# Kernel optimization log

Hardware: AMD Instinct MI355X
Metric: run time of the kernel (lower is better)

Reference implementation:

```python
import jax, jax.numpy as jnp
import numpy as np

EPS = 1e-5
NUM_HEADS = 8
POOL_K = 50
POOL_S = 15
DEPTH = 4


def _conv2d(x, w, b, pad_h, pad_w):
    y = jax.lax.conv_general_dilated(
        x, w, window_strides=(1, 1),
        padding=((pad_h, pad_h), (pad_w, pad_w)),
        dimension_numbers=('NCHW', 'OIHW', 'NCHW'))
    return y + b[None, :, None, None]


def _bn_eval(x, g, b):
    # eval-mode BatchNorm2d with running_mean=0, running_var=1
    s = g / jnp.sqrt(1.0 + EPS)
    return x * s[None, :, None, None] + b[None, :, None, None]


def _layernorm(x, g, b):
    m = x.mean(-1, keepdims=True)
    v = ((x - m) ** 2).mean(-1, keepdims=True)
    return (x - m) / jnp.sqrt(v + EPS) * g + b


def _mha(x, wq, bq, wk, bk, wv, bv, wo, bo):
    B, n, d = x.shape
    def split(h):
        return h.reshape(B, n, NUM_HEADS, -1).transpose(0, 2, 1, 3)  # b h n dk
    q = split(x @ wq.T + bq)
    k = split(x @ wk.T + bk)
    v = split(x @ wv.T + bv)
    dk = q.shape[-1]
    scores = jnp.einsum('bhqd,bhkd->bhqk', q, k) / jnp.sqrt(jnp.float32(dk))
    attn = jax.nn.softmax(scores, axis=-1)
    o = jnp.einsum('bhqk,bhkd->bhqd', attn, v).transpose(0, 2, 1, 3).reshape(B, n, d)
    return o @ wo.T + bo


def _encoder(x, p):
    (g1, b1, g2, b2, wq, bq, wk, bk, wv, bv, wo, bo, f1w, f1b, f2w, f2b) = p
    h = _layernorm(x, g1, b1)
    x = x + _mha(h, wq, bq, wk, bk, wv, bv, wo, bo)
    h = _layernorm(x, g2, b2)
    ff = jax.nn.gelu(h @ f1w.T + f1b, approximate=False) @ f2w.T + f2b
    return x + ff


def _forward(x, tw1, tb1, tw2, tb2, tw3, tb3, tw4, tb4, bn1_g, bn1_b, sw, sb,
             bn2_g, bn2_b, ln1_g, ln1_b, ln2_g, ln2_b, wq, bq, wk, bk, wv, bv,
             wo, bo, f1w, f1b, f2w, f2b, ew, eb, bn3_g, bn3_b, cw, cb):
    B, C, T = x.shape
    xi = x[:, None]  # [B,1,C,T]
    h = jnp.concatenate([
        _conv2d(xi, tw1, tb1, 0, 7),
        _conv2d(xi, tw2, tb2, 0, 12),
        _conv2d(xi, tw3, tb3, 0, 25),
        _conv2d(xi, tw4, tb4, 0, 32)], axis=1)          # [B,D,C,T]
    h = _bn_eval(h, bn1_g, bn1_b)
    h = _conv2d(h, sw, sb, 0, 0)                         # [B,D,1,T]
    h = jax.nn.elu(_bn_eval(h, bn2_g, bn2_b))[:, :, 0]   # [B,D,T]

    npos = (T - POOL_K) // POOL_S + 1
    idx = np.arange(npos)[:, None] * POOL_S + np.arange(POOL_K)  # [n,K]
    win = h[:, :, idx]                                   # [B,D,n,K]
    avg = win.mean(-1)                                   # [B,D,n]
    var = win.var(-1, ddof=1)                            # unbiased, like torch
    vlog = jnp.log(jnp.clip(var, 1e-6, 1e6))
    x1 = avg.transpose(0, 2, 1)                          # [B,n,D]
    x2 = vlog.transpose(0, 2, 1)

    for i in range(DEPTH):
        p = (ln1_g[i], ln1_b[i], ln2_g[i], ln2_b[i], wq[i], bq[i], wk[i], bk[i],
             wv[i], bv[i], wo[i], bo[i], f1w[i], f1b[i], f2w[i], f2b[i])
        x1 = _encoder(x1, p)
        x2 = _encoder(x2, p)

    h = jnp.concatenate([x1[:, :, None, :], x2[:, :, None, :]], axis=2)  # [B,n,2,D]
    h = jax.nn.elu(_bn_eval(_conv2d(h, ew, eb, 0, 0), bn3_g, bn3_b))     # [B,n,1,D]
    return h.reshape(B, -1) @ cw.T + cb


def setup_inputs() -> dict:
    B, C, T, D, n, ff, ncls = 16, 64, 1000, 128, 64, 512, 4
    ks = iter(jax.random.split(jax.random.key(0), 48))
    def nrm(shape, s=0.02):
        return jax.random.normal(next(ks), shape, jnp.float32) * s
    inp = {
        'x': jax.random.normal(next(ks), (B, C, T), jnp.float32),
        'tw1': nrm((D // 4, 1, 1, 15)), 'tb1': jnp.zeros(D // 4),
        'tw2': nrm((D // 4, 1, 1, 25)), 'tb2': jnp.zeros(D // 4),
        'tw3': nrm((D // 4, 1, 1, 51)), 'tb3': jnp.zeros(D // 4),
        'tw4': nrm((D // 4, 1, 1, 65)), 'tb4': jnp.zeros(D // 4),
        'bn1_g': jnp.ones(D), 'bn1_b': jnp.zeros(D),
        'sw': nrm((D, D, C, 1)), 'sb': jnp.zeros(D),
        'bn2_g': jnp.ones(D), 'bn2_b': jnp.zeros(D),
        'ln1_g': jnp.ones((DEPTH, D)), 'ln1_b': jnp.zeros((DEPTH, D)),
        'ln2_g': jnp.ones((DEPTH, D)), 'ln2_b': jnp.zeros((DEPTH, D)),
        'wq': nrm((DEPTH, D, D)), 'bq': jnp.zeros((DEPTH, D)),
        'wk': nrm((DEPTH, D, D)), 'bk': jnp.zeros((DEPTH, D)),
        'wv': nrm((DEPTH, D, D)), 'bv': jnp.zeros((DEPTH, D)),
        'wo': nrm((DEPTH, D, D)), 'bo': jnp.zeros((DEPTH, D)),
        'f1w': nrm((DEPTH, ff, D)), 'f1b': jnp.zeros((DEPTH, ff)),
        'f2w': nrm((DEPTH, D, ff)), 'f2b': jnp.zeros((DEPTH, D)),
        'ew': nrm((n, n, 2, 1)), 'eb': jnp.zeros(n),
        'bn3_g': jnp.ones(n), 'bn3_b': jnp.zeros(n),
        'cw': nrm((ncls, D * n)), 'cb': jnp.zeros(ncls),
    }
    return inp


def reference(x, tw1, tb1, tw2, tb2, tw3, tb3, tw4, tb4, bn1_g, bn1_b, sw, sb,
              bn2_g, bn2_b, ln1_g, ln1_b, ln2_g, ln2_b, wq, bq, wk, bk, wv, bv,
              wo, bo, f1w, f1b, f2w, f2b, ew, eb, bn3_g, bn3_b, cw, cb):
    return _forward(x, tw1, tb1, tw2, tb2, tw3, tb3, tw4, tb4, bn1_g, bn1_b,
                    sw, sb, bn2_g, bn2_b, ln1_g, ln1_b, ln2_g, ln2_b, wq, bq,
                    wk, bk, wv, bv, wo, bo, f1w, f1b, f2w, f2b, ew, eb,
                    bn3_g, bn3_b, cw, cb)
```

## Files before the change

kernel.cpp:

```cpp
#include <hip/hip_runtime.h>
#include <math.h>

typedef unsigned short u16;
typedef __attribute__((ext_vector_type(8))) short frag8;
typedef __attribute__((ext_vector_type(4))) float f32x4;

__device__ __forceinline__ float eluf(float v) { return v > 0.f ? v : expm1f(v); }
__device__ __forceinline__ float geluf(float v) {
  return 0.5f * v * (1.f + erff(v * 0.70710678118654752f));
}
__device__ __forceinline__ u16 f2bf(float f) {
  union { float f; unsigned int i; } v; v.f = f;
  return (u16)((v.i + 0x7fffu + ((v.i >> 16) & 1u)) >> 16);
}

#define BN_S 0.99999500003749969f

__global__ void k_tws1(const float* tw1, const float* tw2, const float* tw3, const float* tw4,
                       const float* tb1, const float* tb2, const float* tb3, const float* tb4,
                       const float* bn1g, const float* bn1b,
                       float* tws1, float* c1) {
  int idx = blockIdx.x * 256 + threadIdx.x;
  if (idx < 8320) {
    int i = idx / 65, u = idx - i * 65;
    int g = i >> 5, il = i & 31;
    const float* tws[4] = {tw1, tw2, tw3, tw4};
    const int P[4] = {7, 12, 25, 32};
    int c = u - 32;
    float s1 = bn1g[i] * BN_S;
    float val = 0.f;
    int p = P[g];
    if (c >= -p && c <= p) val = s1 * tws[g][il * (2 * p + 1) + (c + p)];
    tws1[idx] = val;
  } else if (idx < 8448) {
    int i = idx - 8320;
    int g = i >> 5, il = i & 31;
    const float* tbs[4] = {tb1, tb2, tb3, tb4};
    float s1 = bn1g[i] * BN_S;
    c1[i] = s1 * tbs[g][il] + bn1b[i];
  }
}

__global__ __launch_bounds__(256) void k_weff(const float* __restrict__ sw, const float* __restrict__ sb,
                                              const float* __restrict__ tws1, const float* __restrict__ c1,
                                              u16* __restrict__ Wb, float* __restrict__ biasEff) {
  const int lane = threadIdx.x & 63, wave = threadIdx.x >> 6;
  const int u = blockIdx.x;
  const int o = blockIdx.y * 4 + wave;
  const float* swp = sw + o * 8192 + lane;
  if (u < 65) {
    const float* tp = tws1 + u;
    float a0 = 0.f, a1 = 0.f, a2 = 0.f, a3 = 0.f;
    #pragma unroll 8
    for (int i = 0; i < 128; i += 4) {
      a0 = fmaf(swp[(i + 0) * 64], tp[(i + 0) * 65], a0);
      a1 = fmaf(swp[(i + 1) * 64], tp[(i + 1) * 65], a1);
      a2 = fmaf(swp[(i + 2) * 64], tp[(i + 2) * 65], a2);
      a3 = fmaf(swp[(i + 3) * 64], tp[(i + 3) * 65], a3);
    }
    Wb[(u * 128 + o) * 64 + lane] = f2bf((a0 + a1) + (a2 + a3));
  } else {
    float pa = 0.f;
    #pragma unroll 8
    for (int i = 0; i < 128; i++)
      pa = fmaf(swp[i * 64], c1[i], pa);
    #pragma unroll
    for (int off = 32; off; off >>= 1) pa += __shfl_xor(pa, off);
    if (lane == 0) biasEff[o] = pa + sb[o];
  }
}

__global__ __launch_bounds__(256) void k_conv(const float* __restrict__ x,
                                              const u16* __restrict__ Wb,
                                              const float* __restrict__ biasEff,
                                              const float* __restrict__ bn2g, const float* __restrict__ bn2b,
                                              float* __restrict__ z) {
  __shared__ u16 xs[128 * 88];
  const int tid = threadIdx.x;
  const int t0 = blockIdx.x * 64;
  const int o0 = blockIdx.y * 64;
  const int b  = blockIdx.z;

  #pragma unroll
  for (int i = 0; i < 8; i++) {
    int pos = tid + i * 256;
    int kh = pos >> 5;
    int tt = (pos & 31) * 4;
    int gt = t0 - 32 + tt;
    const float* xp = x + (b * 64 + kh) * 1000;
    float v[4];
    if (gt >= 0 && gt + 3 < 1000) {
      float4 f = *(const float4*)(xp + gt);
      v[0] = f.x; v[1] = f.y; v[2] = f.z; v[3] = f.w;
    } else {
      #pragma unroll
      for (int e = 0; e < 4; e++) { int g2 = gt + e; v[e] = (g2 >= 0 && g2 < 1000) ? xp[g2] : 0.f; }
    }
    #pragma unroll
    for (int e = 0; e < 4; e++) xs[(tt + e) * 88 + kh] = f2bf(v[e]);
  }
  __syncthreads();

  const int lane = tid & 63, wave = tid >> 6;
  const int wt = (wave & 1) * 32;
  const int wo = (wave >> 1) * 32;
  const int m = lane & 15, q = lane >> 4;

  f32x4 acc[2][2];
  #pragma unroll
  for (int i = 0; i < 2; i++)
    #pragma unroll
    for (int j = 0; j < 2; j++) acc[i][j] = (f32x4){0.f, 0.f, 0.f, 0.f};

  #pragma unroll 2
  for (int u = 0; u < 65; u++) {
    frag8 A[2][2], B[2][2];
    #pragma unroll
    for (int tp = 0; tp < 2; tp++)
      #pragma unroll
      for (int kc = 0; kc < 2; kc++)
        A[tp][kc] = *(const frag8*)&xs[(wt + tp * 16 + m + u) * 88 + kc * 32 + q * 8];
    #pragma unroll
    for (int op = 0; op < 2; op++)
      #pragma unroll
      for (int kc = 0; kc < 2; kc++)
        B[op][kc] = *(const frag8*)(Wb + ((u * 128) + o0 + wo + op * 16 + m) * 64 + kc * 32 + q * 8);
    #pragma unroll
    for (int tp = 0; tp < 2; tp++)
      #pragma unroll
      for (int op = 0; op < 2; op++) {
        acc[tp][op] = __builtin_amdgcn_mfma_f32_16x16x32_bf16(A[tp][0], B[op][0], acc[tp][op], 0, 0, 0);
        acc[tp][op] = __builtin_amdgcn_mfma_f32_16x16x32_bf16(A[tp][1], B[op][1], acc[tp][op], 0, 0, 0);
      }
  }

  #pragma unroll
  for (int op = 0; op < 2; op++) {
    int o = o0 + wo + op * 16 + m;
    float s2 = bn2g[o] * BN_S;
    float be = biasEff[o], b2 = bn2b[o];
    #pragma unroll
    for (int tp = 0; tp < 2; tp++) {
      #pragma unroll
      for (int r = 0; r < 4; r++) {
        int t = t0 + wt + tp * 16 + q * 4 + r;
        if (t < 1000)
          z[(b * 128 + o) * 1000 + t] = eluf((acc[tp][op][r] + be) * s2 + b2);
      }
    }
  }
}

__global__ __launch_bounds__(128) void k_pool(const float* __restrict__ z, float* __restrict__ X) {
  int p = blockIdx.x, b = blockIdx.y, o = threadIdx.x;
  const float* zp = z + (b * 128 + o) * 1000 + p * 15;
  float s = 0.f, ss = 0.f;
  #pragma unroll
  for (int k = 0; k < 50; k++) { float v = zp[k]; s += v; ss = fmaf(v, v, ss); }
  float m = s * 0.02f;
  float var = (ss - s * m) * (1.f / 49.f);
  var = fminf(fmaxf(var, 1e-6f), 1e6f);
  X[(b * 64 + p) * 128 + o] = m;
  X[((16 + b) * 64 + p) * 128 + o] = logf(var);
}

__global__ __launch_bounds__(256) void k_cvt6(const float* __restrict__ wq, const float* __restrict__ wk,
                                              const float* __restrict__ wv, const float* __restrict__ wo,
                                              const float* __restrict__ f1w, const float* __restrict__ f2w,
                                              u16* __restrict__ out) {
  int i = blockIdx.x * 256 + threadIdx.x;
  if (i >= 196608) return;
  int fi = i * 4;
  const float* src; int off;
  if      (fi < 65536)  { src = wq;  off = fi; }
  else if (fi < 131072) { src = wk;  off = fi - 65536; }
  else if (fi < 196608) { src = wv;  off = fi - 131072; }
  else if (fi < 262144) { src = wo;  off = fi - 196608; }
  else if (fi < 524288) { src = f1w; off = fi - 262144; }
  else                  { src = f2w; off = fi - 524288; }
  float4 v = *(const float4*)(src + off);
  ushort4 p;
  p.x = f2bf(v.x); p.y = f2bf(v.y); p.z = f2bf(v.z); p.w = f2bf(v.w);
  *(ushort4*)(out + fi) = p;
}

__device__ __forceinline__ void ln128(const float* __restrict__ Xs, u16* __restrict__ Hs,
                                      const float* __restrict__ g, const float* __restrict__ b,
                                      int lane, int wave) {
  float g0 = g[lane], g1 = g[64 + lane], b0 = b[lane], b1 = b[64 + lane];
  #pragma unroll 1
  for (int rr = 0; rr < 8; rr++) {
    int r = wave * 8 + rr;
    float v0 = Xs[r * 132 + lane], v1 = Xs[r * 132 + 64 + lane];
    float s_ = v0 + v1;
    #pragma unroll
    for (int off = 32; off; off >>= 1) s_ += __shfl_xor(s_, off);
    float mn = s_ * (1.f / 128.f);
    float d0 = v0 - mn, d1 = v1 - mn;
    float qq = d0 * d0 + d1 * d1;
    #pragma unroll
    for (int off = 32; off; off >>= 1) qq += __shfl_xor(qq, off);
    float rs = rsqrtf(qq * (1.f / 128.f) + 1e-5f);
    Hs[r * 136 + lane]      = f2bf(d0 * rs * g0 + b0);
    Hs[r * 136 + 64 + lane] = f2bf(d1 * rs * g1 + b1);
  }
}

__device__ __forceinline__ void gemm_tile(const u16* __restrict__ Asrc, int astride,
                                          const u16* __restrict__ Bsrc, int bstride,
                                          int m, int q, f32x4 acc[4]) {
  #pragma unroll
  for (int kc = 0; kc < 4; kc++) {
    frag8 Bf = *(const frag8*)(Bsrc + m * bstride + kc * 32 + q * 8);
    #pragma unroll
    for (int mt = 0; mt < 4; mt++) {
      frag8 Af = *(const frag8*)(Asrc + (mt * 16 + m) * astride + kc * 32 + q * 8);
      acc[mt] = __builtin_amdgcn_mfma_f32_16x16x32_bf16(Af, Bf, acc[mt], 0, 0, 0);
    }
  }
}

__global__ __launch_bounds__(512, 1) void k_enc(float* __restrict__ X,
                                                const u16* __restrict__ Wenc,
                                                const float* __restrict__ ln1g, const float* __restrict__ ln1b,
                                                const float* __restrict__ ln2g, const float* __restrict__ ln2b,
                                                const float* __restrict__ bq, const float* __restrict__ bk,
                                                const float* __restrict__ bv, const float* __restrict__ bo,
                                                const float* __restrict__ f1b, const float* __restrict__ f2b) {
  __shared__ float Xs[64 * 132];
  __shared__ u16   Hs[64 * 136];
  __shared__ float QKV[3 * 64 * 132];
  float* Qs = QKV;
  float* Ks = QKV + 64 * 132;
  float* Vs = QKV + 2 * 64 * 132;
  u16* AOs = (u16*)QKV;
  u16* F1s = (u16*)QKV;

  const int tid = threadIdx.x;
  const int lane = tid & 63, wave = tid >> 6;
  const int m = lane & 15, q = lane >> 4;
  float* Xg = X + blockIdx.x * 64 * 128;

  const u16* WQ  = Wenc;
  const u16* WK  = Wenc + 65536;
  const u16* WV  = Wenc + 131072;
  const u16* WO  = Wenc + 196608;
  const u16* F1W = Wenc + 262144;
  const u16* F2W = Wenc + 524288;

  for (int i = tid; i < 8192; i += 512) Xs[(i >> 7) * 132 + (i & 127)] = Xg[i];
  __syncthreads();

  #pragma unroll 1
  for (int l = 0; l < 4; l++) {
    const u16* wqb  = WQ  + l * 16384;
    const u16* wkb  = WK  + l * 16384;
    const u16* wvb  = WV  + l * 16384;
    const u16* wob  = WO  + l * 16384;
    const u16* f1wb = F1W + l * 65536;
    const u16* f2wb = F2W + l * 65536;
    const int n0 = wave * 16;

    ln128(Xs, Hs, ln1g + l * 128, ln1b + l * 128, lane, wave);
    __syncthreads();

    {
      f32x4 aq[4], ak[4], av[4];
      #pragma unroll
      for (int mt = 0; mt < 4; mt++) { aq[mt] = (f32x4){0,0,0,0}; ak[mt] = (f32x4){0,0,0,0}; av[mt] = (f32x4){0,0,0,0}; }
      gemm_tile(Hs, 136, wqb + n0 * 128, 128, m, q, aq);
      gemm_tile(Hs, 136, wkb + n0 * 128, 128, m, q, ak);
      gemm_tile(Hs, 136, wvb + n0 * 128, 128, m, q, av);
      float bqv = bq[l * 128 + n0 + m];
      float bkv = bk[l * 128 + n0 + m];
      float bvv = bv[l * 128 + n0 + m];
      #pragma unroll
      for (int mt = 0; mt < 4; mt++)
        #pragma unroll
        for (int r = 0; r < 4; r++) {
          int row = mt * 16 + q * 4 + r;
          Qs[row * 132 + n0 + m] = aq[mt][r] + bqv;
          Ks[row * 132 + n0 + m] = ak[mt][r] + bkv;
          Vs[row * 132 + n0 + m] = av[mt][r] + bvv;
        }
    }
    __syncthreads();

    {
      const int h = wave, qr = lane;
      float qv[16];
      {
        const float4* qp = (const float4*)(Qs + qr * 132 + h * 16);
        #pragma unroll
        for (int j = 0; j < 4; j++) {
          float4 t = qp[j];
          qv[j * 4 + 0] = t.x; qv[j * 4 + 1] = t.y; qv[j * 4 + 2] = t.z; qv[j * 4 + 3] = t.w;
        }
      }
      __syncthreads();
      const float* kbase = Ks + h * 16;
      const float* vbase = Vs + h * 16;
      float mrun = -1e30f, lrun = 0.f;
      float o[16];
      #pragma unroll
      for (int j = 0; j < 16; j++) o[j] = 0.f;
      #pragma unroll 1
      for (int k = 0; k < 64; k++) {
        const float4* kp = (const float4*)(kbase + k * 132);
        float4 k0 = kp[0], k1 = kp[1], k2 = kp[2], k3 = kp[3];
        float s0 = qv[0] * k0.x + qv[1] * k0.y + qv[2] * k0.z + qv[3] * k0.w;
        float s1 = qv[4] * k1.x + qv[5] * k1.y + qv[6] * k1.z + qv[7] * k1.w;
        float s2 = qv[8] * k2.x + qv[9] * k2.y + qv[10] * k2.z + qv[11] * k2.w;
        float s3 = qv[12] * k3.x + qv[13] * k3.y + qv[14] * k3.z + qv[15] * k3.w;
        float sc = ((s0 + s1) + (s2 + s3)) * 0.25f;
        float mn = fmaxf(mrun, sc);
        float corr = __expf(mrun - mn);
        float p = __expf(sc - mn);
        lrun = fmaf(lrun, corr, p);
        const float4* vp = (const float4*)(vbase + k * 132);
        float4 v0 = vp[0], v1 = vp[1], v2 = vp[2], v3 = vp[3];
        o[0]  = fmaf(o[0],  corr, p * v0.x); o[1]  = fmaf(o[1],  corr, p * v0.y);
        o[2]  = fmaf(o[2],  corr, p * v0.z); o[3]  = fmaf(o[3],  corr, p * v0.w);
        o[4]  = fmaf(o[4],  corr, p * v1.x); o[5]  = fmaf(o[5],  corr, p * v1.y);
        o[6]  = fmaf(o[6],  corr, p * v1.z); o[7]  = fmaf(o[7],  corr, p * v1.w);
        o[8]  = fmaf(o[8],  corr, p * v2.x); o[9]  = fmaf(o[9],  corr, p * v2.y);
        o[10] = fmaf(o[10], corr, p * v2.z); o[11] = fmaf(o[11], corr, p * v2.w);
        o[12] = fmaf(o[12], corr, p * v3.x); o[13] = fmaf(o[13], corr, p * v3.y);
        o[14] = fmaf(o[14], corr, p * v3.z); o[15] = fmaf(o[15], corr, p * v3.w);
        mrun = mn;
      }
      float inv = 1.f / lrun;
      u16* aop = AOs + qr * 136 + h * 16;
      #pragma unroll
      for (int j = 0; j < 16; j++) aop[j] = f2bf(o[j] * inv);
    }
    __syncthreads();

    {
      f32x4 acc[4];
      #pragma unroll
      for (int mt = 0; mt < 4; mt++) acc[mt] = (f32x4){0,0,0,0};
      gemm_tile(AOs, 136, wob + n0 * 128, 128, m, q, acc);
      float bvv = bo[l * 128 + n0 + m];
      #pragma unroll
      for (int mt = 0; mt < 4; mt++)
        #pragma unroll
        for (int r = 0; r < 4; r++)
          Xs[(mt * 16 + q * 4 + r) * 132 + n0 + m] += acc[mt][r] + bvv;
    }
    __syncthreads();

    ln128(Xs, Hs, ln2g + l * 128, ln2b + l * 128, lane, wave);
    __syncthreads();

    {
      f32x4 acc2[4];
      #pragma unroll
      for (int mt = 0; mt < 4; mt++) acc2[mt] = (f32x4){0,0,0,0};
      #pragma unroll 1
      for (int c = 0; c < 4; c++) {
        f32x4 a1[4];
        #pragma unroll
        for (int mt = 0; mt < 4; mt++) a1[mt] = (f32x4){0,0,0,0};
        gemm_tile(Hs, 136, f1wb + (c * 128 + n0) * 128, 128, m, q, a1);
        float b1v = f1b[l * 512 + c * 128 + n0 + m];
        #pragma unroll
        for (int mt = 0; mt < 4; mt++)
          #pragma unroll
          for (int r = 0; r < 4; r++)
            F1s[(mt * 16 + q * 4 + r) * 136 + n0 + m] = f2bf(geluf(a1[mt][r] + b1v));
        __syncthreads();
        gemm_tile(F1s, 136, f2wb + n0 * 512 + c * 128, 512, m, q, acc2);
        __syncthreads();
      }
      float b2v = f2b[l * 128 + n0 + m];
      #pragma unroll
      for (int mt = 0; mt < 4; mt++)
        #pragma unroll
        for (int r = 0; r < 4; r++)
          Xs[(mt * 16 + q * 4 + r) * 132 + n0 + m] += acc2[mt][r] + b2v;
    }
    __syncthreads();
  }

  for (int i = tid; i < 8192; i += 512) Xg[i] = Xs[(i >> 7) * 132 + (i & 127)];
}

__global__ __launch_bounds__(256) void k_head1(const float* __restrict__ X, const float* __restrict__ ew,
                                               const float* __restrict__ eb, const float* __restrict__ g3,
                                               const float* __restrict__ b3, float* __restrict__ G) {
  __shared__ float Xs[2][8192];
  int b = blockIdx.x, ot = blockIdx.y;
  int tid = threadIdx.x;
  {
    const float4* x1 = (const float4*)(X + b * 8192);
    const float4* x2 = (const float4*)(X + (16 + b) * 8192);
    float4* s1 = (float4*)&Xs[0][0];
    float4* s2 = (float4*)&Xs[1][0];
    for (int i = tid; i < 2048; i += 256) { s1[i] = x1[i]; s2[i] = x2[i]; }
  }
  __syncthreads();
  int w = tid & 127, og = tid >> 7;
  int oc0 = ot * 16 + og * 8;
  float a[8] = {};
  for (int ic = 0; ic < 64; ic++) {
    float x1v = Xs[0][ic * 128 + w], x2v = Xs[1][ic * 128 + w];
    #pragma unroll
    for (int j = 0; j < 8; j++) {
      a[j] = fmaf(ew[((oc0 + j) * 64 + ic) * 2 + 0], x1v, a[j]);
      a[j] = fmaf(ew[((oc0 + j) * 64 + ic) * 2 + 1], x2v, a[j]);
    }
  }
  #pragma unroll
  for (int j = 0; j < 8; j++) {
    int oc = oc0 + j;
    float v = (a[j] + eb[oc]) * (g3[oc] * BN_S) + b3[oc];
    G[(b * 64 + oc) * 128 + w] = eluf(v);
  }
}

__global__ __launch_bounds__(256) void k_head2(const float* __restrict__ G, const float* __restrict__ cw,
                                               const float* __restrict__ cb, float* __restrict__ out) {
  __shared__ float red[256];
  int b = blockIdx.x, c = blockIdx.y, tid = threadIdx.x;
  const float4* g4 = (const float4*)(G + b * 8192);
  const float4* c4 = (const float4*)(cw + c * 8192);
  float p = 0.f;
  for (int i = tid; i < 2048; i += 256) {
    float4 g = g4[i], w = c4[i];
    p += g.x * w.x + g.y * w.y + g.z * w.z + g.w * w.w;
  }
  red[tid] = p;
  __syncthreads();
  for (int s = 128; s > 0; s >>= 1) {
    if (tid < s) red[tid] += red[tid + s];
    __syncthreads();
  }
  if (tid == 0) out[b * 4 + c] = red[0] + cb[c];
}

extern "C" void kernel_launch(void* const* d_in, const int* in_sizes, int n_in,
                              void* d_out, int out_size, void* d_ws, size_t ws_size,
                              hipStream_t stream) {
  const float* x    = (const float*)d_in[0];
  const float* tw1  = (const float*)d_in[1];  const float* tb1 = (const float*)d_in[2];
  const float* tw2  = (const float*)d_in[3];  const float* tb2 = (const float*)d_in[4];
  const float* tw3  = (const float*)d_in[5];  const float* tb3 = (const float*)d_in[6];
  const float* tw4  = (const float*)d_in[7];  const float* tb4 = (const float*)d_in[8];
  const float* bn1g = (const float*)d_in[9];  const float* bn1b = (const float*)d_in[10];
  const float* sw   = (const float*)d_in[11]; const float* sb   = (const float*)d_in[12];
  const float* bn2g = (const float*)d_in[13]; const float* bn2b = (const float*)d_in[14];
  const float* ln1g = (const float*)d_in[15]; const float* ln1b = (const float*)d_in[16];
  const float* ln2g = (const float*)d_in[17]; const float* ln2b = (const float*)d_in[18];
  const float* wq   = (const float*)d_in[19]; const float* bq   = (const float*)d_in[20];
  const float* wk   = (const float*)d_in[21]; const float* bk   = (const float*)d_in[22];
  const float* wv   = (const float*)d_in[23]; const float* bv   = (const float*)d_in[24];
  const float* wo   = (const float*)d_in[25]; const float* bo   = (const float*)d_in[26];
  const float* f1w  = (const float*)d_in[27]; const float* f1b  = (const float*)d_in[28];
  const float* f2w  = (const float*)d_in[29]; const float* f2b  = (const float*)d_in[30];
  const float* ew   = (const float*)d_in[31]; const float* eb   = (const float*)d_in[32];
  const float* g3   = (const float*)d_in[33]; const float* b3   = (const float*)d_in[34];
  const float* cw   = (const float*)d_in[35]; const float* cb   = (const float*)d_in[36];

  float* ws      = (float*)d_ws;
  float* tws1    = ws;
  float* c1      = ws + 8320;
  float* biasEff = ws + 8448;
  u16*   Wb      = (u16*)(ws + 8576);
  float* z       = ws + 541056;
  float* X       = ws + 2589056;
  u16*   Wenc    = (u16*)(ws + 3113344);
  float* G       = z;

  k_cvt6<<<768, 256, 0, stream>>>(wq, wk, wv, wo, f1w, f2w, Wenc);
  k_tws1<<<33, 256, 0, stream>>>(tw1, tw2, tw3, tw4, tb1, tb2, tb3, tb4, bn1g, bn1b, tws1, c1);
  k_weff<<<dim3(66, 32), 256, 0, stream>>>(sw, sb, tws1, c1, Wb, biasEff);
  k_conv<<<dim3(16, 2, 16), 256, 0, stream>>>(x, Wb, biasEff, bn2g, bn2b, z);
  k_pool<<<dim3(64, 16), 128, 0, stream>>>(z, X);

  k_enc<<<32, 512, 0, stream>>>(X, Wenc, ln1g, ln1b, ln2g, ln2b, bq, bk, bv, bo, f1b, f2b);

  k_head1<<<dim3(16, 4), 256, 0, stream>>>(X, ew, eb, g3, b3, G);
  k_head2<<<dim3(16, 4), 256, 0, stream>>>(G, cw, cb, (float*)d_out);
}
```

Before: 420.8 us.

## Restructure weff, conv, pool and encoder kernels for more reuse and overlap

k_weff now stages one output channel's spatial weights and the full temporal table in LDS, computing all 65 taps per block with register blocking. k_conv halves its output-channel tile to double the grid, and k_pool stages z rows in LDS before computing the windowed mean and log-variance. The encoder prefetches weight fragments into registers ahead of the GEMMs, double-buffers the FFN intermediate so a barrier can be dropped, and swaps online softmax for a two-pass softmax with all scores held in registers. These changes target global-load latency, launch occupancy and synchronisation, at the cost of more LDS and register pressure.

```diff
diff --git a/kernel.cpp b/kernel.cpp
--- a/kernel.cpp
+++ b/kernel.cpp
@@ -44,26 +44,51 @@
 __global__ __launch_bounds__(256) void k_weff(const float* __restrict__ sw, const float* __restrict__ sb,
                                               const float* __restrict__ tws1, const float* __restrict__ c1,
                                               u16* __restrict__ Wb, float* __restrict__ biasEff) {
-  const int lane = threadIdx.x & 63, wave = threadIdx.x >> 6;
-  const int u = blockIdx.x;
-  const int o = blockIdx.y * 4 + wave;
-  const float* swp = sw + o * 8192 + lane;
-  if (u < 65) {
-    const float* tp = tws1 + u;
-    float a0 = 0.f, a1 = 0.f, a2 = 0.f, a3 = 0.f;
-    #pragma unroll 8
+  __shared__ float swl[8192];
+  __shared__ float tl[8320];
+  const int tid = threadIdx.x, lane = tid & 63, wave = tid >> 6;
+  const int o = blockIdx.x;
+  for (int idx = tid; idx < 8192; idx += 256) swl[idx] = sw[o * 8192 + idx];
+  for (int idx = tid; idx < 8320; idx += 256) tl[idx] = tws1[idx];
+  __syncthreads();
+
+  #pragma unroll 1
+  for (int j = 0; j < 4; j++) {
+    int u0 = (wave + 4 * j) * 4;
+    float a[4][4];
+    #pragma unroll
+    for (int uu = 0; uu < 4; uu++)
+      #pragma unroll
+      for (int r = 0; r < 4; r++) a[uu][r] = 0.f;
+    #pragma unroll 1
     for (int i = 0; i < 128; i += 4) {
-      a0 = fmaf(swp[(i + 0) * 64], tp[(i + 0) * 65], a0);
-      a1 = fmaf(swp[(i + 1) * 64], tp[(i + 1) * 65], a1);
-      a2 = fmaf(swp[(i + 2) * 64], tp[(i + 2) * 65], a2);
-      a3 = fmaf(swp[(i + 3) * 64], tp[(i + 3) * 65], a3);
-    }
-    Wb[(u * 128 + o) * 64 + lane] = f2bf((a0 + a1) + (a2 + a3));
-  } else {
+      #pragma unroll
+      for (int ii = 0; ii < 4; ii++) {
+        float s = swl[(i + ii) * 64 + lane];
+        #pragma unroll
+        for (int uu = 0; uu < 4; uu++)
+          a[uu][ii] = fmaf(s, tl[(i + ii) * 65 + u0 + uu], a[uu][ii]);
+      }
+    }
+    #pragma unroll
+    for (int uu = 0; uu < 4; uu++)
+      Wb[((u0 + uu) * 128 + o) * 64 + lane] = f2bf((a[uu][0] + a[uu][1]) + (a[uu][2] + a[uu][3]));
+  }
+
+  if (wave == 0) {
+    float a[4] = {0.f, 0.f, 0.f, 0.f};
+    #pragma unroll 1
+    for (int i = 0; i < 128; i += 4) {
+      #pragma unroll
+      for (int ii = 0; ii < 4; ii++)
+        a[ii] = fmaf(swl[(i + ii) * 64 + lane], tl[(i + ii) * 65 + 64], a[ii]);
+    }
+    Wb[(64 * 128 + o) * 64 + lane] = f2bf((a[0] + a[1]) + (a[2] + a[3]));
+  } else if (wave == 1) {
     float pa = 0.f;
     #pragma unroll 8
     for (int i = 0; i < 128; i++)
-      pa = fmaf(swp[i * 64], c1[i], pa);
+      pa = fmaf(swl[i * 64 + lane], c1[i], pa);
     #pragma unroll
     for (int off = 32; off; off >>= 1) pa += __shfl_xor(pa, off);
     if (lane == 0) biasEff[o] = pa + sb[o];
@@ -78,7 +103,7 @@
   __shared__ u16 xs[128 * 88];
   const int tid = threadIdx.x;
   const int t0 = blockIdx.x * 64;
-  const int o0 = blockIdx.y * 64;
+  const int o0 = blockIdx.y * 32;
   const int b  = blockIdx.z;
 
   #pragma unroll
@@ -103,40 +128,33 @@
 
   const int lane = tid & 63, wave = tid >> 6;
   const int wt = (wave & 1) * 32;
-  const int wo = (wave >> 1) * 32;
+  const int wo = (wave >> 1) * 16;
   const int m = lane & 15, q = lane >> 4;
 
-  f32x4 acc[2][2];
+  f32x4 acc[2];
   #pragma unroll
-  for (int i = 0; i < 2; i++)
-    #pragma unroll
-    for (int j = 0; j < 2; j++) acc[i][j] = (f32x4){0.f, 0.f, 0.f, 0.f};
+  for (int i = 0; i < 2; i++) acc[i] = (f32x4){0.f, 0.f, 0.f, 0.f};
 
   #pragma unroll 2
   for (int u = 0; u < 65; u++) {
-    frag8 A[2][2], B[2][2];
+    frag8 A[2][2], B[2];
     #pragma unroll
     for (int tp = 0; tp < 2; tp++)
       #pragma unroll
       for (int kc = 0; kc < 2; kc++)
         A[tp][kc] = *(const frag8*)&xs[(wt + tp * 16 + m + u) * 88 + kc * 32 + q * 8];
     #pragma unroll
-    for (int op = 0; op < 2; op++)
-      #pragma unroll
-      for (int kc = 0; kc < 2; kc++)
-        B[op][kc] = *(const frag8*)(Wb + ((u * 128) + o0 + wo + op * 16 + m) * 64 + kc * 32 + q * 8);
-    #pragma unroll
-    for (int tp = 0; tp < 2; tp++)
-      #pragma unroll
-      for (int op = 0; op < 2; op++) {
-        acc[tp][op] = __builtin_amdgcn_mfma_f32_16x16x32_bf16(A[tp][0], B[op][0], acc[tp][op], 0, 0, 0);
-        acc[tp][op] = __builtin_amdgcn_mfma_f32_16x16x32_bf16(A[tp][1], B[op][1], acc[tp][op], 0, 0, 0);
-      }
-  }
-
-  #pragma unroll
-  for (int op = 0; op < 2; op++) {
-    int o = o0 + wo + op * 16 + m;
+    for (int kc = 0; kc < 2; kc++)
+      B[kc] = *(const frag8*)(Wb + ((u * 128) + o0 + wo + m) * 64 + kc * 32 + q * 8);
+    #pragma unroll
+    for (int tp = 0; tp < 2; tp++) {
+      acc[tp] = __builtin_amdgcn_mfma_f32_16x16x32_bf16(A[tp][0], B[0], acc[tp], 0, 0, 0);
+      acc[tp] = __builtin_amdgcn_mfma_f32_16x16x32_bf16(A[tp][1], B[1], acc[tp], 0, 0, 0);
+    }
+  }
+
+  {
+    int o = o0 + wo + m;
     float s2 = bn2g[o] * BN_S;
     float be = biasEff[o], b2 = bn2b[o];
     #pragma unroll
@@ -145,23 +163,38 @@
       for (int r = 0; r < 4; r++) {
         int t = t0 + wt + tp * 16 + q * 4 + r;
         if (t < 1000)
-          z[(b * 128 + o) * 1000 + t] = eluf((acc[tp][op][r] + be) * s2 + b2);
+          z[(b * 128 + o) * 1000 + t] = eluf((acc[tp][r] + be) * s2 + b2);
       }
     }
   }
 }
 
-__global__ __launch_bounds__(128) void k_pool(const float* __restrict__ z, float* __restrict__ X) {
-  int p = blockIdx.x, b = blockIdx.y, o = threadIdx.x;
-  const float* zp = z + (b * 128 + o) * 1000 + p * 15;
-  float s = 0.f, ss = 0.f;
-  #pragma unroll
-  for (int k = 0; k < 50; k++) { float v = zp[k]; s += v; ss = fmaf(v, v, ss); }
-  float m = s * 0.02f;
-  float var = (ss - s * m) * (1.f / 49.f);
-  var = fminf(fmaxf(var, 1e-6f), 1e6f);
-  X[(b * 64 + p) * 128 + o] = m;
-  X[((16 + b) * 64 + p) * 128 + o] = logf(var);
+__global__ __launch_bounds__(256) void k_pool(const float* __restrict__ z, float* __restrict__ X) {
+  __shared__ float zl[16 * 1001];
+  int b = blockIdx.x, og = blockIdx.y;
+  int tid = threadIdx.x;
+  const float* zb = z + (b * 128 + og * 16) * 1000;
+  #pragma unroll 1
+  for (int r = 0; r < 16; r++)
+    for (int c = tid; c < 1000; c += 256) zl[r * 1001 + c] = zb[r * 1000 + c];
+  __syncthreads();
+
+  int ol = tid & 15;
+  int pb = tid >> 4;
+  #pragma unroll 1
+  for (int pass = 0; pass < 4; pass++) {
+    int p = pb + pass * 16;
+    const float* zp = zl + ol * 1001 + p * 15;
+    float s = 0.f, ss = 0.f;
+    #pragma unroll
+    for (int k = 0; k < 50; k++) { float v = zp[k]; s += v; ss = fmaf(v, v, ss); }
+    float m = s * 0.02f;
+    float var = (ss - s * m) * (1.f / 49.f);
+    var = fminf(fmaxf(var, 1e-6f), 1e6f);
+    int o = og * 16 + ol;
+    X[(b * 64 + p) * 128 + o] = m;
+    X[((16 + b) * 64 + p) * 128 + o] = logf(var);
+  }
 }
 
 __global__ __launch_bounds__(256) void k_cvt6(const float* __restrict__ wq, const float* __restrict__ wk,
@@ -188,7 +221,7 @@
                                       const float* __restrict__ g, const float* __restrict__ b,
                                       int lane, int wave) {
   float g0 = g[lane], g1 = g[64 + lane], b0 = b[lane], b1 = b[64 + lane];
-  #pragma unroll 1
+  #pragma unroll
   for (int rr = 0; rr < 8; rr++) {
     int r = wave * 8 + rr;
     float v0 = Xs[r * 132 + lane], v1 = Xs[r * 132 + 64 + lane];
@@ -206,16 +239,14 @@
   }
 }
 
-__device__ __forceinline__ void gemm_tile(const u16* __restrict__ Asrc, int astride,
-                                          const u16* __restrict__ Bsrc, int bstride,
-                                          int m, int q, f32x4 acc[4]) {
+__device__ __forceinline__ void gemm_pref(const u16* __restrict__ Asrc, int astride,
+                                          const frag8 Bf[4], int m, int q, f32x4 acc[4]) {
   #pragma unroll
   for (int kc = 0; kc < 4; kc++) {
-    frag8 Bf = *(const frag8*)(Bsrc + m * bstride + kc * 32 + q * 8);
     #pragma unroll
     for (int mt = 0; mt < 4; mt++) {
       frag8 Af = *(const frag8*)(Asrc + (mt * 16 + m) * astride + kc * 32 + q * 8);
-      acc[mt] = __builtin_amdgcn_mfma_f32_16x16x32_bf16(Af, Bf, acc[mt], 0, 0, 0);
+      acc[mt] = __builtin_amdgcn_mfma_f32_16x16x32_bf16(Af, Bf[kc], acc[mt], 0, 0, 0);
     }
   }
 }
@@ -233,12 +264,14 @@
   float* Qs = QKV;
   float* Ks = QKV + 64 * 132;
   float* Vs = QKV + 2 * 64 * 132;
-  u16* AOs = (u16*)QKV;
-  u16* F1s = (u16*)QKV;
+  u16* AOs  = Hs;
+  u16* F1a  = (u16*)QKV;
+  u16* F1b_ = (u16*)QKV + 64 * 136;
 
   const int tid = threadIdx.x;
   const int lane = tid & 63, wave = tid >> 6;
   const int m = lane & 15, q = lane >> 4;
+  const int n0 = wave * 16;
   float* Xg = X + blockIdx.x * 64 * 128;
 
   const u16* WQ  = Wenc;
@@ -259,18 +292,29 @@
     const u16* wob  = WO  + l * 16384;
     const u16* f1wb = F1W + l * 65536;
     const u16* f2wb = F2W + l * 65536;
-    const int n0 = wave * 16;
+
+    frag8 fq[4], fk[4], fv[4];
+    #pragma unroll
+    for (int kc = 0; kc < 4; kc++) {
+      fq[kc] = *(const frag8*)(wqb + (n0 + m) * 128 + kc * 32 + q * 8);
+      fk[kc] = *(const frag8*)(wkb + (n0 + m) * 128 + kc * 32 + q * 8);
+      fv[kc] = *(const frag8*)(wvb + (n0 + m) * 128 + kc * 32 + q * 8);
+    }
 
     ln128(Xs, Hs, ln1g + l * 128, ln1b + l * 128, lane, wave);
     __syncthreads();
 
+    frag8 fo[4];
+    #pragma unroll
+    for (int kc = 0; kc < 4; kc++)
+      fo[kc] = *(const frag8*)(wob + (n0 + m) * 128 + kc * 32 + q * 8);
     {
       f32x4 aq[4], ak[4], av[4];
       #pragma unroll
       for (int mt = 0; mt < 4; mt++) { aq[mt] = (f32x4){0,0,0,0}; ak[mt] = (f32x4){0,0,0,0}; av[mt] = (f32x4){0,0,0,0}; }
-      gemm_tile(Hs, 136, wqb + n0 * 128, 128, m, q, aq);
-      gemm_tile(Hs, 136, wkb + n0 * 128, 128, m, q, ak);
-      gemm_tile(Hs, 136, wvb + n0 * 128, 128, m, q, av);
+      gemm_pref(Hs, 136, fq, m, q, aq);
+      gemm_pref(Hs, 136, fk, m, q, ak);
+      gemm_pref(Hs, 136, fv, m, q, av);
       float bqv = bq[l * 128 + n0 + m];
       float bkv = bk[l * 128 + n0 + m];
       float bvv = bv[l * 128 + n0 + m];
@@ -286,6 +330,10 @@
     }
     __syncthreads();
 
+    frag8 f1f[4];
+    #pragma unroll
+    for (int kc = 0; kc < 4; kc++)
+      f1f[kc] = *(const frag8*)(f1wb + (n0 + m) * 128 + kc * 32 + q * 8);
     {
       const int h = wave, qr = lane;
       float qv[16];
@@ -297,39 +345,49 @@
           qv[j * 4 + 0] = t.x; qv[j * 4 + 1] = t.y; qv[j * 4 + 2] = t.z; qv[j * 4 + 3] = t.w;
         }
       }
-      __syncthreads();
       const float* kbase = Ks + h * 16;
       const float* vbase = Vs + h * 16;
-      float mrun = -1e30f, lrun = 0.f;
+      float s_[64];
+      float m0 = -1e30f, m1 = -1e30f, m2 = -1e30f, m3 = -1e30f;
+      #pragma unroll
+      for (int k4 = 0; k4 < 64; k4 += 4) {
+        #pragma unroll
+        for (int e = 0; e < 4; e++) {
+          const float4* kp = (const float4*)(kbase + (k4 + e) * 132);
+          float4 k0 = kp[0], k1 = kp[1], k2 = kp[2], k3 = kp[3];
+          float d0 = qv[0] * k0.x + qv[1] * k0.y + qv[2] * k0.z + qv[3] * k0.w;
+          float d1 = qv[4] * k1.x + qv[5] * k1.y + qv[6] * k1.z + qv[7] * k1.w;
+          float d2 = qv[8] * k2.x + qv[9] * k2.y + qv[10] * k2.z + qv[11] * k2.w;
+          float d3 = qv[12] * k3.x + qv[13] * k3.y + qv[14] * k3.z + qv[15] * k3.w;
+          float sc = ((d0 + d1) + (d2 + d3)) * 0.25f;
+          s_[k4 + e] = sc;
+          if (e == 0) m0 = fmaxf(m0, sc);
+          else if (e == 1) m1 = fmaxf(m1, sc);
+          else if (e == 2) m2 = fmaxf(m2, sc);
+          else m3 = fmaxf(m3, sc);
+        }
+      }
+      float mx = fmaxf(fmaxf(m0, m1), fmaxf(m2, m3));
+      float l_ = 0.f;
       float o[16];
       #pragma unroll
       for (int j = 0; j < 16; j++) o[j] = 0.f;
-      #pragma unroll 1
+      #pragma unroll
       for (int k = 0; k < 64; k++) {
-        const float4* kp = (const float4*)(kbase + k * 132);
-        float4 k0 = kp[0], k1 = kp[1], k2 = kp[2], k3 = kp[3];
-        float s0 = qv[0] * k0.x + qv[1] * k0.y + qv[2] * k0.z + qv[3] * k0.w;
-        float s1 = qv[4] * k1.x + qv[5] * k1.y + qv[6] * k1.z + qv[7] * k1.w;
-        float s2 = qv[8] * k2.x + qv[9] * k2.y + qv[10] * k2.z + qv[11] * k2.w;
-        float s3 = qv[12] * k3.x + qv[13] * k3.y + qv[14] * k3.z + qv[15] * k3.w;
-        float sc = ((s0 + s1) + (s2 + s3)) * 0.25f;
-        float mn = fmaxf(mrun, sc);
-        float corr = __expf(mrun - mn);
-        float p = __expf(sc - mn);
-        lrun = fmaf(lrun, corr, p);
+        float p = __expf(s_[k] - mx);
+        l_ += p;
         const float4* vp = (const float4*)(vbase + k * 132);
         float4 v0 = vp[0], v1 = vp[1], v2 = vp[2], v3 = vp[3];
-        o[0]  = fmaf(o[0],  corr, p * v0.x); o[1]  = fmaf(o[1],  corr, p * v0.y);
-        o[2]  = fmaf(o[2],  corr, p * v0.z); o[3]  = fmaf(o[3],  corr, p * v0.w);
-        o[4]  = fmaf(o[4],  corr, p * v1.x); o[5]  = fmaf(o[5],  corr, p * v1.y);
-        o[6]  = fmaf(o[6],  corr, p * v1.z); o[7]  = fmaf(o[7],  corr, p * v1.w);
-        o[8]  = fmaf(o[8],  corr, p * v2.x); o[9]  = fmaf(o[9],  corr, p * v2.y);
-        o[10] = fmaf(o[10], corr, p * v2.z); o[11] = fmaf(o[11], corr, p * v2.w);
-        o[12] = fmaf(o[12], corr, p * v3.x); o[13] = fmaf(o[13], corr, p * v3.y);
-        o[14] = fmaf(o[14], corr, p * v3.z); o[15] = fmaf(o[15], corr, p * v3.w);
-        mrun = mn;
+        o[0]  = fmaf(p, v0.x, o[0]);  o[1]  = fmaf(p, v0.y, o[1]);
+        o[2]  = fmaf(p, v0.z, o[2]);  o[3]  = fmaf(p, v0.w, o[3]);
+        o[4]  = fmaf(p, v1.x, o[4]);  o[5]  = fmaf(p, v1.y, o[5]);
+        o[6]  = fmaf(p, v1.z, o[6]);  o[7]  = fmaf(p, v1.w, o[7]);
+        o[8]  = fmaf(p, v2.x, o[8]);  o[9]  = fmaf(p, v2.y, o[9]);
+        o[10] = fmaf(p, v2.z, o[10]); o[11] = fmaf(p, v2.w, o[11]);
+        o[12] = fmaf(p, v3.x, o[12]); o[13] = fmaf(p, v3.y, o[13]);
+        o[14] = fmaf(p, v3.z, o[14]); o[15] = fmaf(p, v3.w, o[15]);
       }
-      float inv = 1.f / lrun;
+      float inv = 1.f / l_;
       u16* aop = AOs + qr * 136 + h * 16;
       #pragma unroll
       for (int j = 0; j < 16; j++) aop[j] = f2bf(o[j] * inv);
@@ -337,16 +395,16 @@
     __syncthreads();
 
     {
-      f32x4 acc[4];
-      #pragma unroll
-      for (int mt = 0; mt < 4; mt++) acc[mt] = (f32x4){0,0,0,0};
-      gemm_tile(AOs, 136, wob + n0 * 128, 128, m, q, acc);
-      float bvv = bo[l * 128 + n0 + m];
+      f32x4 ao4[4];
+      #pragma unroll
+      for (int mt = 0; mt < 4; mt++) ao4[mt] = (f32x4){0,0,0,0};
+      gemm_pref(AOs, 136, fo, m, q, ao4);
+      float bov = bo[l * 128 + n0 + m];
       #pragma unroll
       for (int mt = 0; mt < 4; mt++)
         #pragma unroll
         for (int r = 0; r < 4; r++)
-          Xs[(mt * 16 + q * 4 + r) * 132 + n0 + m] += acc[mt][r] + bvv;
+          Xs[(mt * 16 + q * 4 + r) * 132 + n0 + m] += ao4[mt][r] + bov;
     }
     __syncthreads();
 
@@ -359,19 +417,30 @@
       for (int mt = 0; mt < 4; mt++) acc2[mt] = (f32x4){0,0,0,0};
       #pragma unroll 1
       for (int c = 0; c < 4; c++) {
-        f32x4 a1[4];
-        #pragma unroll
-        for (int mt = 0; mt < 4; mt++) a1[mt] = (f32x4){0,0,0,0};
-        gemm_tile(Hs, 136, f1wb + (c * 128 + n0) * 128, 128, m, q, a1);
-        float b1v = f1b[l * 512 + c * 128 + n0 + m];
-        #pragma unroll
-        for (int mt = 0; mt < 4; mt++)
+        frag8 f2f[4];
+        #pragma unroll
+        for (int kc = 0; kc < 4; kc++)
+          f2f[kc] = *(const frag8*)(f2wb + (n0 + m) * 512 + c * 128 + kc * 32 + q * 8);
+        u16* F1c = (c & 1) ? F1b_ : F1a;
+        {
+          f32x4 a1[4];
           #pragma unroll
-          for (int r = 0; r < 4; r++)
-            F1s[(mt * 16 + q * 4 + r) * 136 + n0 + m] = f2bf(geluf(a1[mt][r] + b1v));
+          for (int mt = 0; mt < 4; mt++) a1[mt] = (f32x4){0,0,0,0};
+          gemm_pref(Hs, 136, f1f, m, q, a1);
+          float b1v = f1b[l * 512 + c * 128 + n0 + m];
+          #pragma unroll
+          for (int mt = 0; mt < 4; mt++)
+            #pragma unroll
+            for (int r = 0; r < 4; r++)
+              F1c[(mt * 16 + q * 4 + r) * 136 + n0 + m] = f2bf(geluf(a1[mt][r] + b1v));
+        }
         __syncthreads();
-        gemm_tile(F1s, 136, f2wb + n0 * 512 + c * 128, 512, m, q, acc2);
-        __syncthreads();
+        if (c < 3) {
+          #pragma unroll
+          for (int kc = 0; kc < 4; kc++)
+            f1f[kc] = *(const frag8*)(f1wb + ((c + 1) * 128 + n0 + m) * 128 + kc * 32 + q * 8);
+        }
+        gemm_pref(F1c, 136, f2f, m, q, acc2);
       }
       float b2v = f2b[l * 128 + n0 + m];
       #pragma unroll
@@ -474,9 +543,9 @@
 
   k_cvt6<<<768, 256, 0, stream>>>(wq, wk, wv, wo, f1w, f2w, Wenc);
   k_tws1<<<33, 256, 0, stream>>>(tw1, tw2, tw3, tw4, tb1, tb2, tb3, tb4, bn1g, bn1b, tws1, c1);
-  k_weff<<<dim3(66, 32), 256, 0, stream>>>(sw, sb, tws1, c1, Wb, biasEff);
-  k_conv<<<dim3(16, 2, 16), 256, 0, stream>>>(x, Wb, biasEff, bn2g, bn2b, z);
-  k_pool<<<dim3(64, 16), 128, 0, stream>>>(z, X);
+  k_weff<<<128, 256, 0, stream>>>(sw, sb, tws1, c1, Wb, biasEff);
+  k_conv<<<dim3(16, 4, 16), 256, 0, stream>>>(x, Wb, biasEff, bn2g, bn2b, z);
+  k_pool<<<dim3(16, 8), 256, 0, stream>>>(z, X);
 
   k_enc<<<32, 512, 0, stream>>>(X, Wenc, ln1g, ln1b, ln2g, ln2b, bq, bk, bv, bo, f1b, f2b);
 
```

Result: faster. 404.8 us (-3.8%).
